# Kernel optimization log

Hardware: AMD Instinct MI355X
Metric: run time of the kernel (lower is better)

## Reference

```python
import jax, jax.numpy as jnp
import numpy as np

D_MODEL = 1024
NUM_HEADS = 16
HEAD_DIM = D_MODEL // NUM_HEADS


def setup_inputs() -> dict:
    key = jax.random.key(0)
    ks = jax.random.split(key, 10)
    B, T, D = 2, 2048, D_MODEL
    scale = 1.0 / np.sqrt(D)
    inp = {
        "x": jax.random.normal(ks[0], (B, T, D), dtype=jnp.float32),
        "mask": jax.random.randint(ks[1], (B, T), 0, 2).astype(jnp.int32),
        "Wq": jax.random.normal(ks[2], (D, D), dtype=jnp.float32) * scale,
        "bq": jnp.zeros((D,), dtype=jnp.float32),
        "Wk": jax.random.normal(ks[3], (D, D), dtype=jnp.float32) * scale,
        "bk": jnp.zeros((D,), dtype=jnp.float32),
        "Wv": jax.random.normal(ks[4], (D, D), dtype=jnp.float32) * scale,
        "bv": jnp.zeros((D,), dtype=jnp.float32),
        "Wo": jax.random.normal(ks[5], (D, D), dtype=jnp.float32) * scale,
        "bo": jnp.zeros((D,), dtype=jnp.float32),
    }
    return inp


def reference(x, mask, Wq, bq, Wk, bk, Wv, bv, Wo, bo):
    B, T, D = x.shape
    H, Hd = NUM_HEADS, HEAD_DIM
    # torch Linear: y = x @ W.T + b
    Q = (x @ Wq.T + bq).reshape(B, T, H, Hd).transpose(0, 2, 1, 3)  # [B,H,T,Hd]
    K = (x @ Wk.T + bk).reshape(B, T, H, Hd).transpose(0, 2, 1, 3)
    V = (x @ Wv.T + bv).reshape(B, T, H, Hd).transpose(0, 2, 1, 3)
    scores = jnp.einsum("bhqd,bhkd->bhqk", Q, K) / jnp.sqrt(jnp.float32(Hd))
    # key padding mask: 1=valid, 0=pad -> -inf on padded keys
    key_pad = (mask == 0)[:, None, None, :]  # [B,1,1,T]
    scores = jnp.where(key_pad, -jnp.inf, scores)
    attn = jax.nn.softmax(scores, axis=-1)  # [B,H,T,T]
    # dropout p=0.0 (inference): identity
    context = jnp.einsum("bhqk,bhkd->bhqd", attn, V)  # [B,H,T,Hd]
    context = context.transpose(0, 2, 1, 3).reshape(B, T, D)
    output = context @ Wo.T + bo
    return (output, attn)
```

## Files before the change

kernel.cpp:

```cpp
#include <hip/hip_runtime.h>
#include <math.h>

#define SEQ   2048
#define BATCH 2
#define DM    1024
#define NH    16
#define HD    64
#define MTOT  (BATCH*SEQ)
#define NQSZ  ((size_t)BATCH*NH*SEQ*HD)

typedef __bf16 bf16_t;
typedef __bf16 bf16x4 __attribute__((ext_vector_type(4)));
typedef __bf16 bf16x8 __attribute__((ext_vector_type(8)));
typedef float  f32x4  __attribute__((ext_vector_type(4)));

typedef __attribute__((address_space(1))) void glob_void;
typedef __attribute__((address_space(3))) void lds_void;
#define GL2LDS(gp, lp) __builtin_amdgcn_global_load_lds( \
    (glob_void*)(gp), (lds_void*)(lp), 16, 0, 0)

#define SCL 0.18033688f

__global__ __launch_bounds__(256)
void cvt_all(const float* __restrict__ x, const float* __restrict__ wq,
             const float* __restrict__ wk, const float* __restrict__ wv,
             const float* __restrict__ wo, bf16_t* __restrict__ xb,
             bf16_t* __restrict__ wb)
{
    const int gid = blockIdx.x * 256 + threadIdx.x;
    const size_t idx = (size_t)gid * 4;
    const float* src;
    bf16_t* dst;
    if (idx < (size_t)MTOT * DM) {
        src = x + idx; dst = xb + idx;
    } else {
        const size_t widx = idx - (size_t)MTOT * DM;
        const int w = (int)(widx >> 20);
        const size_t off = widx & ((1u << 20) - 1);
        const float* s = w == 0 ? wq : (w == 1 ? wk : (w == 2 ? wv : wo));
        src = s + off; dst = wb + widx;
    }
    float4 f = *(const float4*)src;
    bf16x4 h;
    h.x = (__bf16)f.x; h.y = (__bf16)f.y; h.z = (__bf16)f.z; h.w = (__bf16)f.w;
    *(bf16x4*)dst = h;
}

template<int MODE>
__global__ __launch_bounds__(256)
void gemm_bt(const bf16_t* __restrict__ A, const bf16_t* __restrict__ W,
             const float* __restrict__ b0p, const float* __restrict__ b1p,
             const float* __restrict__ b2p, void* __restrict__ outp,
             bf16_t* __restrict__ vtp)
{
    __shared__ __align__(16) bf16_t As[128 * 32];
    __shared__ __align__(16) bf16_t Bs[128 * 32];
    const int n0 = blockIdx.x * 128, m0 = blockIdx.y * 128;
    const int tid = threadIdx.x, lane = tid & 63, wave = tid >> 6;
    const int wm = (wave >> 1) * 64, wn = (wave & 1) * 64;
    const int srow = wave * 32 + (lane >> 2);
    const int scol = (lane & 3) * 8;
    const int fr = lane & 15, fk = (lane >> 4) * 8;
    const bf16_t* gA = &A[(size_t)(m0 + srow) * DM + scol];
    const bf16_t* gB = &W[(size_t)(n0 + srow) * DM + scol];
    bf16_t* lA = &As[wave * 1024];
    bf16_t* lB = &Bs[wave * 1024];
    f32x4 acc[4][4] = {};
    for (int k0 = 0; k0 < DM; k0 += 32) {
        GL2LDS(gA,            lA);
        GL2LDS(gA + 16 * DM,  lA + 16 * 32);
        GL2LDS(gB,            lB);
        GL2LDS(gB + 16 * DM,  lB + 16 * 32);
        gA += 32; gB += 32;
        __syncthreads();
        bf16x8 af[4], bv[4];
        #pragma unroll
        for (int mi = 0; mi < 4; ++mi)
            af[mi] = *(const bf16x8*)&As[(wm + mi * 16 + fr) * 32 + fk];
        #pragma unroll
        for (int ni = 0; ni < 4; ++ni)
            bv[ni] = *(const bf16x8*)&Bs[(wn + ni * 16 + fr) * 32 + fk];
        #pragma unroll
        for (int mi = 0; mi < 4; ++mi)
            #pragma unroll
            for (int ni = 0; ni < 4; ++ni)
                acc[mi][ni] = __builtin_amdgcn_mfma_f32_16x16x32_bf16(af[mi], bv[ni], acc[mi][ni], 0, 0, 0);
        __syncthreads();
    }
    const int cr = (lane >> 4) * 4, cc = lane & 15;
    const int which = n0 >> 10;
    #pragma unroll
    for (int mi = 0; mi < 4; ++mi) {
        #pragma unroll
        for (int ni = 0; ni < 4; ++ni) {
            const int n = n0 + wn + ni * 16 + cc;
            float bn;
            if (MODE == 0) {
                const int nn = n & 1023;
                const float* bp = which == 0 ? b0p : (which == 1 ? b1p : b2p);
                bn = bp[nn];
            } else {
                bn = b0p[n];
            }
            if (MODE == 0 && which == 2) {
                const int m_ = m0 + wm + mi * 16 + cr;
                const int b_ = m_ >> 11, t0 = m_ & (SEQ - 1);
                const int nn = n & 1023, h = nn >> 6, hd = nn & 63;
                bf16x4 pk;
                pk.x = (__bf16)(acc[mi][ni][0] + bn);
                pk.y = (__bf16)(acc[mi][ni][1] + bn);
                pk.z = (__bf16)(acc[mi][ni][2] + bn);
                pk.w = (__bf16)(acc[mi][ni][3] + bn);
                *(bf16x4*)&vtp[(((size_t)(b_ * NH + h)) * HD + hd) * SEQ + t0] = pk;
            } else {
                #pragma unroll
                for (int v = 0; v < 4; ++v) {
                    const int m = m0 + wm + mi * 16 + cr + v;
                    const float val = acc[mi][ni][v] + bn;
                    if (MODE == 0) {
                        const int nn = n & 1023;
                        const int b_ = m >> 11, t = m & (SEQ - 1);
                        const int h = nn >> 6, hd = nn & 63;
                        ((bf16_t*)outp)[(size_t)which * NQSZ +
                            (((size_t)(b_ * NH + h)) * SEQ + t) * HD + hd] = (__bf16)val;
                    } else {
                        ((float*)outp)[(size_t)m * DM + n] = val;
                    }
                }
            }
        }
    }
}

__global__ __launch_bounds__(256, 2)
void fused_attn(const bf16_t* __restrict__ Q, const bf16_t* __restrict__ K,
                const bf16_t* __restrict__ Vt, const int* __restrict__ mask,
                float* __restrict__ attn, bf16_t* __restrict__ ctxb)
{
    __shared__ __align__(16) float  P32[8192];
    __shared__ __align__(16) bf16_t Ksd[2 * 8192];
    __shared__ __align__(16) bf16_t Vs[8192];

    const int bid = blockIdx.x;
    const int grp = bid & 7, g2 = bid >> 3;
    const int bh = grp * 4 + (g2 >> 4);
    const int qt = g2 & 15;
    const int b = bh >> 4, h = bh & 15;
    const int q0 = qt * 128;

    const bf16_t* Qb  = Q  + (size_t)bh * SEQ * HD + (size_t)q0 * HD;
    const bf16_t* Kb  = K  + (size_t)bh * SEQ * HD;
    const bf16_t* Vtb = Vt + (size_t)bh * HD * SEQ;
    const int*    mb  = mask + b * SEQ;
    float*        Ab  = attn + (size_t)bh * SEQ * SEQ;

    const int tid = threadIdx.x, lane = tid & 63, wave = tid >> 6;
    const int wm = wave * 32;
    const int fr = lane & 15, fg = lane >> 4, fk = fg * 8;
    const int cr = fg * 4, cc = fr;

    int koff[4], voff[4];
    #pragma unroll
    for (int i = 0; i < 4; ++i) {
        const int seg = wave * 4 + i;
        const int k5 = (lane & 3) * 8;
        koff[i] = ((seg & 7) * 16 + (lane >> 2)) * HD + (seg >> 3) * 32 + k5;
        voff[i] = ((seg & 3) * 16 + (lane >> 2)) * SEQ + (seg >> 2) * 32 + k5;
    }
    const int segb = wave * 4 * 512;

    bf16_t* Qstage = (bf16_t*)P32;
    #pragma unroll
    for (int i = 0; i < 4; ++i) GL2LDS(Qb + koff[i], Qstage + segb + i * 512);
    #pragma unroll
    for (int i = 0; i < 4; ++i) GL2LDS(Kb + koff[i], Ksd + segb + i * 512);
    __syncthreads();

    bf16x8 qf[2][2];
    #pragma unroll
    for (int mi = 0; mi < 2; ++mi)
        #pragma unroll
        for (int c = 0; c < 2; ++c)
            qf[mi][c] = *(const bf16x8*)&Qstage[c * 4096 + (wm + mi * 16 + fr) * 32 + fk];

    float rs[2][4] = {};

    int cur = 0;
    for (int t = 0; t < 16; ++t) {
        const int kt0 = t * 128;
        if (t < 15) {
            const bf16_t* ns = Kb + (size_t)(kt0 + 128) * HD;
            bf16_t* nd = Ksd + (cur ^ 1) * 8192 + segb;
            #pragma unroll
            for (int i = 0; i < 4; ++i) GL2LDS(ns + koff[i], nd + i * 512);
        }
        const bf16_t* Kc = Ksd + cur * 8192;
        float ma[8];
        #pragma unroll
        for (int ni = 0; ni < 8; ++ni)
            ma[ni] = mb[kt0 + ni * 16 + cc] ? 0.f : -1e30f;
        f32x4 acc[2][8] = {};
        #pragma unroll
        for (int ni = 0; ni < 8; ++ni) {
            bf16x8 b0 = *(const bf16x8*)&Kc[(ni * 16 + fr) * 32 + fk];
            bf16x8 b1 = *(const bf16x8*)&Kc[4096 + (ni * 16 + fr) * 32 + fk];
            acc[0][ni] = __builtin_amdgcn_mfma_f32_16x16x32_bf16(qf[0][0], b0, acc[0][ni], 0, 0, 0);
            acc[1][ni] = __builtin_amdgcn_mfma_f32_16x16x32_bf16(qf[1][0], b0, acc[1][ni], 0, 0, 0);
            acc[0][ni] = __builtin_amdgcn_mfma_f32_16x16x32_bf16(qf[0][1], b1, acc[0][ni], 0, 0, 0);
            acc[1][ni] = __builtin_amdgcn_mfma_f32_16x16x32_bf16(qf[1][1], b1, acc[1][ni], 0, 0, 0);
        }
        #pragma unroll
        for (int mi = 0; mi < 2; ++mi)
            #pragma unroll
            for (int v = 0; v < 4; ++v) {
                float s = 0.f;
                #pragma unroll
                for (int ni = 0; ni < 8; ++ni)
                    s += exp2f(acc[mi][ni][v] * SCL + ma[ni]);
                rs[mi][v] += s;
            }
        __syncthreads();
        cur ^= 1;
    }

    float invl[2][4];
    #pragma unroll
    for (int mi = 0; mi < 2; ++mi)
        #pragma unroll
        for (int v = 0; v < 4; ++v) {
            float ls = rs[mi][v];
            ls += __shfl_xor(ls, 1);
            ls += __shfl_xor(ls, 2);
            ls += __shfl_xor(ls, 4);
            ls += __shfl_xor(ls, 8);
            invl[mi][v] = 1.0f / ls;
        }

    f32x4 oac[2][4] = {};
    float* Pw = P32 + wave * 2048;
    cur = 0;
    #pragma unroll
    for (int i = 0; i < 4; ++i) GL2LDS(Kb + koff[i], Ksd + segb + i * 512);
    __syncthreads();
    for (int t = 0; t < 16; ++t) {
        const int kt0 = t * 128;
        if (t < 15) {
            const bf16_t* ns = Kb + (size_t)(kt0 + 128) * HD;
            bf16_t* nd = Ksd + (cur ^ 1) * 8192 + segb;
            #pragma unroll
            for (int i = 0; i < 4; ++i) GL2LDS(ns + koff[i], nd + i * 512);
        }
        {
            const bf16_t* vsrc = Vtb + kt0;
            #pragma unroll
            for (int i = 0; i < 4; ++i) GL2LDS(vsrc + voff[i], Vs + segb + i * 512);
        }
        const bf16_t* Kc = Ksd + cur * 8192;
        float ma[8];
        #pragma unroll
        for (int ni = 0; ni < 8; ++ni)
            ma[ni] = mb[kt0 + ni * 16 + cc] ? 0.f : -1e30f;
        f32x4 acc[2][8] = {};
        #pragma unroll
        for (int ni = 0; ni < 8; ++ni) {
            bf16x8 b0 = *(const bf16x8*)&Kc[(ni * 16 + fr) * 32 + fk];
            bf16x8 b1 = *(const bf16x8*)&Kc[4096 + (ni * 16 + fr) * 32 + fk];
            acc[0][ni] = __builtin_amdgcn_mfma_f32_16x16x32_bf16(qf[0][0], b0, acc[0][ni], 0, 0, 0);
            acc[1][ni] = __builtin_amdgcn_mfma_f32_16x16x32_bf16(qf[1][0], b0, acc[1][ni], 0, 0, 0);
            acc[0][ni] = __builtin_amdgcn_mfma_f32_16x16x32_bf16(qf[0][1], b1, acc[0][ni], 0, 0, 0);
            acc[1][ni] = __builtin_amdgcn_mfma_f32_16x16x32_bf16(qf[1][1], b1, acc[1][ni], 0, 0, 0);
        }
        bf16x8 pf[2][4];
        const int xkg = fr >> 2;
        #pragma unroll
        for (int mi = 0; mi < 2; ++mi) {
            #pragma unroll
            for (int ni = 0; ni < 8; ++ni) {
                const int c = ni * 16 + cc;
                #pragma unroll
                for (int v = 0; v < 4; ++v) {
                    const int r = cr + v;
                    float p = exp2f(acc[mi][ni][v] * SCL + ma[ni]) * invl[mi][v];
                    Pw[r * 128 + ((((c >> 2) ^ fg) << 2) | (c & 3))] = p;
                }
            }
            float* arow = &Ab[(size_t)(q0 + wm + mi * 16 + fr) * SEQ + kt0 + fg * 8];
            #pragma unroll
            for (int ks = 0; ks < 4; ++ks) {
                const int g0 = ks * 8 + fg * 2;
                f32x4 pa = *(const f32x4*)&Pw[fr * 128 + ((g0 ^ xkg) << 2)];
                f32x4 pb = *(const f32x4*)&Pw[fr * 128 + (((g0 + 1) ^ xkg) << 2)];
                *(f32x4*)&arow[ks * 32]     = pa;
                *(f32x4*)&arow[ks * 32 + 4] = pb;
                bf16x8 f;
                f[0] = (__bf16)pa[0]; f[1] = (__bf16)pa[1];
                f[2] = (__bf16)pa[2]; f[3] = (__bf16)pa[3];
                f[4] = (__bf16)pb[0]; f[5] = (__bf16)pb[1];
                f[6] = (__bf16)pb[2]; f[7] = (__bf16)pb[3];
                pf[mi][ks] = f;
            }
        }
        __syncthreads();
        #pragma unroll
        for (int ks = 0; ks < 4; ++ks) {
            #pragma unroll
            for (int ni = 0; ni < 4; ++ni) {
                bf16x8 vf = *(const bf16x8*)&Vs[ks * 2048 + (ni * 16 + fr) * 32 + fk];
                oac[0][ni] = __builtin_amdgcn_mfma_f32_16x16x32_bf16(pf[0][ks], vf, oac[0][ni], 0, 0, 0);
                oac[1][ni] = __builtin_amdgcn_mfma_f32_16x16x32_bf16(pf[1][ks], vf, oac[1][ni], 0, 0, 0);
            }
        }
        __syncthreads();
        cur ^= 1;
    }
    #pragma unroll
    for (int mi = 0; mi < 2; ++mi) {
        #pragma unroll
        for (int ni = 0; ni < 4; ++ni) {
            #pragma unroll
            for (int v = 0; v < 4; ++v) {
                const int t = q0 + wm + mi * 16 + cr + v;
                ctxb[((size_t)b * SEQ + t) * DM + h * HD + ni * 16 + cc] = (__bf16)oac[mi][ni][v];
            }
        }
    }
}

extern "C" void kernel_launch(void* const* d_in, const int* in_sizes, int n_in,
                              void* d_out, int out_size, void* d_ws, size_t ws_size,
                              hipStream_t stream)
{
    const float* x   = (const float*)d_in[0];
    const int*  mask = (const int*)d_in[1];
    const float* Wq  = (const float*)d_in[2];
    const float* bq  = (const float*)d_in[3];
    const float* Wk  = (const float*)d_in[4];
    const float* bk  = (const float*)d_in[5];
    const float* Wv  = (const float*)d_in[6];
    const float* bv  = (const float*)d_in[7];
    const float* Wo  = (const float*)d_in[8];
    const float* bo  = (const float*)d_in[9];

    float* out  = (float*)d_out;
    float* attn = out + (size_t)BATCH * SEQ * DM;

    const size_t NX = (size_t)MTOT * DM;
    const size_t NW = (size_t)DM * DM;

    bf16_t* xb   = (bf16_t*)d_ws;
    bf16_t* Wqb  = xb + NX;
    bf16_t* Wob  = Wqb + 3 * NW;
    bf16_t* Qb   = Wob + NW;
    bf16_t* Kb   = Qb + NQSZ;
    bf16_t* Vt   = Kb + NQSZ;
    bf16_t* ctxb = Vt + NQSZ;

    cvt_all<<<dim3((NX + 4 * NW) / 1024), 256, 0, stream>>>(
        x, Wq, Wk, Wv, Wo, xb, Wqb);

    gemm_bt<0><<<dim3(3 * DM / 128, MTOT / 128), 256, 0, stream>>>(
        xb, Wqb, bq, bk, bv, Qb, Vt);

    fused_attn<<<dim3(BATCH * NH * (SEQ / 128)), 256, 0, stream>>>(
        Qb, Kb, Vt, mask, attn, ctxb);

    gemm_bt<1><<<dim3(DM / 128, MTOT / 128), 256, 0, stream>>>(
        ctxb, Wob, bo, bo, bo, out, nullptr);
}
```

Before: 759.4 us.

## Restructure attention to per-wave 16-row tiles reading K/V directly from global

Rewrites the fused attention kernel so each wave owns 16 query rows and loads K and V fragments straight from global memory instead of staging shared K/V tiles in LDS with block-wide barriers. It computes S^T (K as the A operand) so probabilities land in a row-contiguous layout for vectorized attn stores. It precomputes a float mask in the conversion kernel and uses multiplication instead of an additive -inf bias. Block count doubles and occupancy is raised to 4, which removes syncthreads and cuts LDS use but gives up K/V reuse across waves and relies on L2/L1 caching for repeated K/V reads.

```diff
diff --git a/kernel.cpp b/kernel.cpp
--- a/kernel.cpp
+++ b/kernel.cpp
@@ -20,15 +20,29 @@
     (glob_void*)(gp), (lds_void*)(lp), 16, 0, 0)
 
 #define SCL 0.18033688f
+#define MFMA __builtin_amdgcn_mfma_f32_16x16x32_bf16
 
 __global__ __launch_bounds__(256)
 void cvt_all(const float* __restrict__ x, const float* __restrict__ wq,
              const float* __restrict__ wk, const float* __restrict__ wv,
-             const float* __restrict__ wo, bf16_t* __restrict__ xb,
-             bf16_t* __restrict__ wb)
+             const float* __restrict__ wo, const int* __restrict__ mask,
+             bf16_t* __restrict__ xb, bf16_t* __restrict__ wb,
+             float* __restrict__ maskf)
 {
     const int gid = blockIdx.x * 256 + threadIdx.x;
     const size_t idx = (size_t)gid * 4;
+    const size_t nmain = (size_t)MTOT * DM + 4 * (size_t)DM * DM;
+    if (idx >= nmain) {
+        const size_t moff = idx - nmain;
+        if (moff < MTOT) {
+            int4 mi = *(const int4*)(mask + moff);
+            float4 mo;
+            mo.x = mi.x ? 1.f : 0.f; mo.y = mi.y ? 1.f : 0.f;
+            mo.z = mi.z ? 1.f : 0.f; mo.w = mi.w ? 1.f : 0.f;
+            *(float4*)(maskf + moff) = mo;
+        }
+        return;
+    }
     const float* src;
     bf16_t* dst;
     if (idx < (size_t)MTOT * DM) {
@@ -84,7 +98,7 @@
         for (int mi = 0; mi < 4; ++mi)
             #pragma unroll
             for (int ni = 0; ni < 4; ++ni)
-                acc[mi][ni] = __builtin_amdgcn_mfma_f32_16x16x32_bf16(af[mi], bv[ni], acc[mi][ni], 0, 0, 0);
+                acc[mi][ni] = MFMA(af[mi], bv[ni], acc[mi][ni], 0, 0, 0);
         __syncthreads();
     }
     const int cr = (lane >> 4) * 4, cc = lane & 15;
@@ -132,196 +146,101 @@
     }
 }
 
-__global__ __launch_bounds__(256, 2)
+__global__ __launch_bounds__(256, 4)
 void fused_attn(const bf16_t* __restrict__ Q, const bf16_t* __restrict__ K,
-                const bf16_t* __restrict__ Vt, const int* __restrict__ mask,
+                const bf16_t* __restrict__ Vt, const float* __restrict__ maskf,
                 float* __restrict__ attn, bf16_t* __restrict__ ctxb)
 {
-    __shared__ __align__(16) float  P32[8192];
-    __shared__ __align__(16) bf16_t Ksd[2 * 8192];
-    __shared__ __align__(16) bf16_t Vs[8192];
+    __shared__ __align__(16) bf16_t Pl[4][16 * 136];
 
     const int bid = blockIdx.x;
-    const int grp = bid & 7, g2 = bid >> 3;
-    const int bh = grp * 4 + (g2 >> 4);
-    const int qt = g2 & 15;
+    const int g2 = bid >> 3;
+    const int bh = (bid & 7) * 4 + (g2 >> 5);
+    const int qt = g2 & 31;
     const int b = bh >> 4, h = bh & 15;
-    const int q0 = qt * 128;
-
-    const bf16_t* Qb  = Q  + (size_t)bh * SEQ * HD + (size_t)q0 * HD;
+
+    const int tid = threadIdx.x, lane = tid & 63, wave = tid >> 6;
+    const int fr = lane & 15, fg = lane >> 4;
+    const int qbase = qt * 64 + wave * 16;
+
+    const bf16_t* Qb  = Q  + ((size_t)bh * SEQ + qbase) * HD;
     const bf16_t* Kb  = K  + (size_t)bh * SEQ * HD;
     const bf16_t* Vtb = Vt + (size_t)bh * HD * SEQ;
-    const int*    mb  = mask + b * SEQ;
-    float*        Ab  = attn + (size_t)bh * SEQ * SEQ;
-
-    const int tid = threadIdx.x, lane = tid & 63, wave = tid >> 6;
-    const int wm = wave * 32;
-    const int fr = lane & 15, fg = lane >> 4, fk = fg * 8;
-    const int cr = fg * 4, cc = fr;
-
-    int koff[4], voff[4];
-    #pragma unroll
-    for (int i = 0; i < 4; ++i) {
-        const int seg = wave * 4 + i;
-        const int k5 = (lane & 3) * 8;
-        koff[i] = ((seg & 7) * 16 + (lane >> 2)) * HD + (seg >> 3) * 32 + k5;
-        voff[i] = ((seg & 3) * 16 + (lane >> 2)) * SEQ + (seg >> 2) * 32 + k5;
-    }
-    const int segb = wave * 4 * 512;
-
-    bf16_t* Qstage = (bf16_t*)P32;
-    #pragma unroll
-    for (int i = 0; i < 4; ++i) GL2LDS(Qb + koff[i], Qstage + segb + i * 512);
-    #pragma unroll
-    for (int i = 0; i < 4; ++i) GL2LDS(Kb + koff[i], Ksd + segb + i * 512);
-    __syncthreads();
-
-    bf16x8 qf[2][2];
-    #pragma unroll
-    for (int mi = 0; mi < 2; ++mi)
-        #pragma unroll
-        for (int c = 0; c < 2; ++c)
-            qf[mi][c] = *(const bf16x8*)&Qstage[c * 4096 + (wm + mi * 16 + fr) * 32 + fk];
-
-    float rs[2][4] = {};
-
-    int cur = 0;
+    const float*  mfp = maskf + b * SEQ;
+    float*        Ab  = attn + ((size_t)bh * SEQ + qbase) * SEQ;
+
+    bf16x8 qf[2];
+    qf[0] = *(const bf16x8*)&Qb[(size_t)fr * HD + fg * 8];
+    qf[1] = *(const bf16x8*)&Qb[(size_t)fr * HD + 32 + fg * 8];
+
+    float rs = 0.f;
     for (int t = 0; t < 16; ++t) {
         const int kt0 = t * 128;
-        if (t < 15) {
-            const bf16_t* ns = Kb + (size_t)(kt0 + 128) * HD;
-            bf16_t* nd = Ksd + (cur ^ 1) * 8192 + segb;
-            #pragma unroll
-            for (int i = 0; i < 4; ++i) GL2LDS(ns + koff[i], nd + i * 512);
-        }
-        const bf16_t* Kc = Ksd + cur * 8192;
-        float ma[8];
-        #pragma unroll
-        for (int ni = 0; ni < 8; ++ni)
-            ma[ni] = mb[kt0 + ni * 16 + cc] ? 0.f : -1e30f;
-        f32x4 acc[2][8] = {};
-        #pragma unroll
-        for (int ni = 0; ni < 8; ++ni) {
-            bf16x8 b0 = *(const bf16x8*)&Kc[(ni * 16 + fr) * 32 + fk];
-            bf16x8 b1 = *(const bf16x8*)&Kc[4096 + (ni * 16 + fr) * 32 + fk];
-            acc[0][ni] = __builtin_amdgcn_mfma_f32_16x16x32_bf16(qf[0][0], b0, acc[0][ni], 0, 0, 0);
-            acc[1][ni] = __builtin_amdgcn_mfma_f32_16x16x32_bf16(qf[1][0], b0, acc[1][ni], 0, 0, 0);
-            acc[0][ni] = __builtin_amdgcn_mfma_f32_16x16x32_bf16(qf[0][1], b1, acc[0][ni], 0, 0, 0);
-            acc[1][ni] = __builtin_amdgcn_mfma_f32_16x16x32_bf16(qf[1][1], b1, acc[1][ni], 0, 0, 0);
-        }
-        #pragma unroll
-        for (int mi = 0; mi < 2; ++mi)
-            #pragma unroll
-            for (int v = 0; v < 4; ++v) {
-                float s = 0.f;
-                #pragma unroll
-                for (int ni = 0; ni < 8; ++ni)
-                    s += exp2f(acc[mi][ni][v] * SCL + ma[ni]);
-                rs[mi][v] += s;
-            }
-        __syncthreads();
-        cur ^= 1;
-    }
-
-    float invl[2][4];
-    #pragma unroll
-    for (int mi = 0; mi < 2; ++mi)
-        #pragma unroll
-        for (int v = 0; v < 4; ++v) {
-            float ls = rs[mi][v];
-            ls += __shfl_xor(ls, 1);
-            ls += __shfl_xor(ls, 2);
-            ls += __shfl_xor(ls, 4);
-            ls += __shfl_xor(ls, 8);
-            invl[mi][v] = 1.0f / ls;
-        }
-
-    f32x4 oac[2][4] = {};
-    float* Pw = P32 + wave * 2048;
-    cur = 0;
-    #pragma unroll
-    for (int i = 0; i < 4; ++i) GL2LDS(Kb + koff[i], Ksd + segb + i * 512);
-    __syncthreads();
+        f32x4 acc[8] = {};
+        #pragma unroll
+        for (int kmi = 0; kmi < 8; ++kmi) {
+            const bf16_t* kr = &Kb[(size_t)(kt0 + kmi * 16 + fr) * HD + fg * 8];
+            bf16x8 a0 = *(const bf16x8*)kr;
+            bf16x8 a1 = *(const bf16x8*)(kr + 32);
+            acc[kmi] = MFMA(a0, qf[0], acc[kmi], 0, 0, 0);
+            acc[kmi] = MFMA(a1, qf[1], acc[kmi], 0, 0, 0);
+        }
+        #pragma unroll
+        for (int kmi = 0; kmi < 8; ++kmi) {
+            f32x4 mf = *(const f32x4*)&mfp[kt0 + kmi * 16 + fg * 4];
+            #pragma unroll
+            for (int v = 0; v < 4; ++v)
+                rs += exp2f(acc[kmi][v] * SCL) * mf[v];
+        }
+    }
+    rs += __shfl_xor(rs, 16);
+    rs += __shfl_xor(rs, 32);
+    const float invl = 1.0f / rs;
+
+    f32x4 oac[4] = {};
+    bf16_t* Pw = &Pl[wave][0];
     for (int t = 0; t < 16; ++t) {
         const int kt0 = t * 128;
-        if (t < 15) {
-            const bf16_t* ns = Kb + (size_t)(kt0 + 128) * HD;
-            bf16_t* nd = Ksd + (cur ^ 1) * 8192 + segb;
-            #pragma unroll
-            for (int i = 0; i < 4; ++i) GL2LDS(ns + koff[i], nd + i * 512);
-        }
-        {
-            const bf16_t* vsrc = Vtb + kt0;
-            #pragma unroll
-            for (int i = 0; i < 4; ++i) GL2LDS(vsrc + voff[i], Vs + segb + i * 512);
-        }
-        const bf16_t* Kc = Ksd + cur * 8192;
-        float ma[8];
-        #pragma unroll
-        for (int ni = 0; ni < 8; ++ni)
-            ma[ni] = mb[kt0 + ni * 16 + cc] ? 0.f : -1e30f;
-        f32x4 acc[2][8] = {};
-        #pragma unroll
-        for (int ni = 0; ni < 8; ++ni) {
-            bf16x8 b0 = *(const bf16x8*)&Kc[(ni * 16 + fr) * 32 + fk];
-            bf16x8 b1 = *(const bf16x8*)&Kc[4096 + (ni * 16 + fr) * 32 + fk];
-            acc[0][ni] = __builtin_amdgcn_mfma_f32_16x16x32_bf16(qf[0][0], b0, acc[0][ni], 0, 0, 0);
-            acc[1][ni] = __builtin_amdgcn_mfma_f32_16x16x32_bf16(qf[1][0], b0, acc[1][ni], 0, 0, 0);
-            acc[0][ni] = __builtin_amdgcn_mfma_f32_16x16x32_bf16(qf[0][1], b1, acc[0][ni], 0, 0, 0);
-            acc[1][ni] = __builtin_amdgcn_mfma_f32_16x16x32_bf16(qf[1][1], b1, acc[1][ni], 0, 0, 0);
-        }
-        bf16x8 pf[2][4];
-        const int xkg = fr >> 2;
-        #pragma unroll
-        for (int mi = 0; mi < 2; ++mi) {
-            #pragma unroll
-            for (int ni = 0; ni < 8; ++ni) {
-                const int c = ni * 16 + cc;
-                #pragma unroll
-                for (int v = 0; v < 4; ++v) {
-                    const int r = cr + v;
-                    float p = exp2f(acc[mi][ni][v] * SCL + ma[ni]) * invl[mi][v];
-                    Pw[r * 128 + ((((c >> 2) ^ fg) << 2) | (c & 3))] = p;
-                }
+        f32x4 acc[8] = {};
+        #pragma unroll
+        for (int kmi = 0; kmi < 8; ++kmi) {
+            const bf16_t* kr = &Kb[(size_t)(kt0 + kmi * 16 + fr) * HD + fg * 8];
+            bf16x8 a0 = *(const bf16x8*)kr;
+            bf16x8 a1 = *(const bf16x8*)(kr + 32);
+            acc[kmi] = MFMA(a0, qf[0], acc[kmi], 0, 0, 0);
+            acc[kmi] = MFMA(a1, qf[1], acc[kmi], 0, 0, 0);
+        }
+        #pragma unroll
+        for (int kmi = 0; kmi < 8; ++kmi) {
+            f32x4 mf = *(const f32x4*)&mfp[kt0 + kmi * 16 + fg * 4];
+            f32x4 p;
+            #pragma unroll
+            for (int v = 0; v < 4; ++v)
+                p[v] = exp2f(acc[kmi][v] * SCL) * mf[v] * invl;
+            *(f32x4*)&Ab[(size_t)fr * SEQ + kt0 + kmi * 16 + fg * 4] = p;
+            bf16x4 pb;
+            pb.x = (__bf16)p[0]; pb.y = (__bf16)p[1];
+            pb.z = (__bf16)p[2]; pb.w = (__bf16)p[3];
+            *(bf16x4*)&Pw[fr * 136 + kmi * 16 + fg * 4] = pb;
+        }
+        #pragma unroll
+        for (int ks = 0; ks < 4; ++ks) {
+            bf16x8 pf = *(const bf16x8*)&Pw[fr * 136 + ks * 32 + fg * 8];
+            #pragma unroll
+            for (int ni = 0; ni < 4; ++ni) {
+                bf16x8 vf = *(const bf16x8*)&Vtb[(size_t)(ni * 16 + fr) * SEQ +
+                                                 kt0 + ks * 32 + fg * 8];
+                oac[ni] = MFMA(pf, vf, oac[ni], 0, 0, 0);
             }
-            float* arow = &Ab[(size_t)(q0 + wm + mi * 16 + fr) * SEQ + kt0 + fg * 8];
-            #pragma unroll
-            for (int ks = 0; ks < 4; ++ks) {
-                const int g0 = ks * 8 + fg * 2;
-                f32x4 pa = *(const f32x4*)&Pw[fr * 128 + ((g0 ^ xkg) << 2)];
-                f32x4 pb = *(const f32x4*)&Pw[fr * 128 + (((g0 + 1) ^ xkg) << 2)];
-                *(f32x4*)&arow[ks * 32]     = pa;
-                *(f32x4*)&arow[ks * 32 + 4] = pb;
-                bf16x8 f;
-                f[0] = (__bf16)pa[0]; f[1] = (__bf16)pa[1];
-                f[2] = (__bf16)pa[2]; f[3] = (__bf16)pa[3];
-                f[4] = (__bf16)pb[0]; f[5] = (__bf16)pb[1];
-                f[6] = (__bf16)pb[2]; f[7] = (__bf16)pb[3];
-                pf[mi][ks] = f;
-            }
-        }
-        __syncthreads();
-        #pragma unroll
-        for (int ks = 0; ks < 4; ++ks) {
-            #pragma unroll
-            for (int ni = 0; ni < 4; ++ni) {
-                bf16x8 vf = *(const bf16x8*)&Vs[ks * 2048 + (ni * 16 + fr) * 32 + fk];
-                oac[0][ni] = __builtin_amdgcn_mfma_f32_16x16x32_bf16(pf[0][ks], vf, oac[0][ni], 0, 0, 0);
-                oac[1][ni] = __builtin_amdgcn_mfma_f32_16x16x32_bf16(pf[1][ks], vf, oac[1][ni], 0, 0, 0);
-            }
-        }
-        __syncthreads();
-        cur ^= 1;
+        }
     }
     #pragma unroll
-    for (int mi = 0; mi < 2; ++mi) {
-        #pragma unroll
-        for (int ni = 0; ni < 4; ++ni) {
-            #pragma unroll
-            for (int v = 0; v < 4; ++v) {
-                const int t = q0 + wm + mi * 16 + cr + v;
-                ctxb[((size_t)b * SEQ + t) * DM + h * HD + ni * 16 + cc] = (__bf16)oac[mi][ni][v];
-            }
+    for (int ni = 0; ni < 4; ++ni) {
+        #pragma unroll
+        for (int v = 0; v < 4; ++v) {
+            const int tq = qbase + fg * 4 + v;
+            ctxb[((size_t)b * SEQ + tq) * DM + h * HD + ni * 16 + fr] =
+                (__bf16)oac[ni][v];
         }
     }
 }
@@ -354,15 +273,16 @@
     bf16_t* Kb   = Qb + NQSZ;
     bf16_t* Vt   = Kb + NQSZ;
     bf16_t* ctxb = Vt + NQSZ;
-
-    cvt_all<<<dim3((NX + 4 * NW) / 1024), 256, 0, stream>>>(
-        x, Wq, Wk, Wv, Wo, xb, Wqb);
+    float*  maskf = (float*)(ctxb + NQSZ);
+
+    cvt_all<<<dim3((NX + 4 * NW) / 1024 + 4), 256, 0, stream>>>(
+        x, Wq, Wk, Wv, Wo, mask, xb, Wqb, maskf);
 
     gemm_bt<0><<<dim3(3 * DM / 128, MTOT / 128), 256, 0, stream>>>(
         xb, Wqb, bq, bk, bv, Qb, Vt);
 
-    fused_attn<<<dim3(BATCH * NH * (SEQ / 128)), 256, 0, stream>>>(
-        Qb, Kb, Vt, mask, attn, ctxb);
+    fused_attn<<<dim3(BATCH * NH * (SEQ / 64)), 256, 0, stream>>>(
+        Qb, Kb, Vt, maskf, attn, ctxb);
 
     gemm_bt<1><<<dim3(DM / 128, MTOT / 128), 256, 0, stream>>>(
         ctxb, Wob, bo, bo, bo, out, nullptr);
```

Result: slower. 977.4 us (+28.7%).
